# Kernel optimization log

Measured on AMD Instinct MI355X. Metric: run time of the kernel, lower is better.

## Reference

```python
import jax, jax.numpy as jnp
import numpy as np

BETA = 0.9
NORM_EPS = 1e-12  # torch F.normalize default eps


def _sqdist(u, v):
    # ||u||^2 + ||v||^2 - 2 u v^T  (matches module's dist())
    return (u ** 2).sum(1, keepdims=True) + (v ** 2).sum(1) - 2.0 * u @ v.T


def setup_inputs() -> dict:
    key = jax.random.key(0)
    k1, k2 = jax.random.split(key)
    z = jax.random.normal(k1, (16, 4096, 128), dtype=jnp.float32)
    # codebook: unit-norm rows (Hypersphere.random_uniform init)
    w = jax.random.normal(k2, (1024, 128), dtype=jnp.float32)
    emb_w = w / jnp.linalg.norm(w, axis=1, keepdims=True)
    return {"z": z, "emb_w": emb_w}


def reference(z, emb_w):
    B, N, D = z.shape
    n_e = emb_w.shape[0]
    zf = z.reshape(-1, D)  # [B*N, D]

    # codebook self-distances + stats
    cd = _sqdist(emb_w, emb_w)                      # [n_e, n_e]
    min_distance = jnp.sort(cd, axis=0)[1]          # kthvalue(cd, 2, dim=0)
    mean_cb_distance = min_distance.mean()
    mean_cb_variance = jnp.var(cd, axis=1, ddof=1).mean()  # torch.var unbiased

    # quantisation: argmin over codebook
    d = _sqdist(zf, emb_w)                          # [B*N, n_e]
    idx = jnp.argmin(d, axis=1)                     # [B*N]
    z_q = emb_w[idx].reshape(z.shape)               # [B, N, D]

    # F.normalize default dim=1 applied to the 3D tensor -> normalize over N axis
    zn = z_q / jnp.maximum(jnp.linalg.norm(z_q, axis=1, keepdims=True), NORM_EPS)

    sg = jax.lax.stop_gradient
    # legacy loss
    loss = jnp.mean((sg(z_q) - z) ** 2) + BETA * jnp.mean((z_q - sg(z)) ** 2)

    # straight-through estimator
    z_q_st = z + sg(z_q - z)

    # sampled_idx buffer of length B*n_e, scatter 1s at the encoding indices
    sampled_idx = jnp.zeros(B * n_e, dtype=z.dtype).at[idx].set(1.0).reshape(B, n_e)

    si = idx.reshape(B, N)
    return (z_q_st, loss, sampled_idx, idx.reshape(B, -1),
            mean_cb_variance, mean_cb_distance, si, zn)
```

## Files before the change

### kernel.cpp

```cpp
#include <hip/hip_runtime.h>
#include <math.h>

#define D       128
#define NE      1024
#define NROWS   65536
#define NB      16

#define OUT_ZQ    0
#define OUT_LOSS  8388608
#define OUT_SAMP  8388609
#define OUT_IDX   8404993
#define OUT_VAR   8470529
#define OUT_DIST  8470530
#define OUT_SI    8470531
#define OUT_ZN    8536067

#define SCR       8536068
#define SCR_WL    (SCR + 65536)
#define SCR_CNT   (SCR + 131072)
#define SCR_LIST  (SCR + 131073)

#define WS_IDX    0
#define WS_WW     65536
#define WS_FLAGS  66560
#define WS_MIN2   67584
#define WS_VAR    68608
#define WS_LOSSP  69632
#define WS_COLSQP 70144
#define WS_COLSQ  135680

#define MARGIN 2e-3f

typedef __attribute__((ext_vector_type(8))) short s16x8;
typedef __attribute__((ext_vector_type(4))) float f32x4;

#define GLDS16(gp, lp)                                                        \
  __builtin_amdgcn_global_load_lds(                                           \
      (const __attribute__((address_space(1))) unsigned int*)(gp),            \
      (__attribute__((address_space(3))) unsigned int*)(lp), 16, 0, 0)

__device__ __forceinline__ unsigned short f2bf(float f) {
  unsigned int u = __float_as_uint(f);
  return (unsigned short)((u + 0x7FFFu + ((u >> 16) & 1u)) >> 16);
}
__device__ __forceinline__ float bf2f(unsigned short h) {
  return __uint_as_float(((unsigned int)h) << 16);
}

__device__ __forceinline__ float npsq_sum128(const float* p) {
  float a[8];
#pragma unroll
  for (int m = 0; m < 8; ++m) a[m] = __fmul_rn(p[m], p[m]);
  for (int k = 8; k < 128; k += 8) {
#pragma unroll
    for (int m = 0; m < 8; ++m) a[m] = __fadd_rn(a[m], __fmul_rn(p[k + m], p[k + m]));
  }
  float s01 = __fadd_rn(a[0], a[1]);
  float s23 = __fadd_rn(a[2], a[3]);
  float s45 = __fadd_rn(a[4], a[5]);
  float s67 = __fadd_rn(a[6], a[7]);
  return __fadd_rn(__fadd_rn(s01, s23), __fadd_rn(s45, s67));
}

__global__ __launch_bounds__(256) void k_wsplit(const float* __restrict__ w,
                                                float* __restrict__ out,
                                                float* __restrict__ ws) {
  int u = blockIdx.x * 256 + threadIdx.x;
  int c = u >> 4, j = u & 15;
  const float4* p = (const float4*)(w + c * D + j * 8);
  float4 f0 = p[0], f1 = p[1];
  float ff[8] = {f0.x, f0.y, f0.z, f0.w, f1.x, f1.y, f1.z, f1.w};
  s16x8 h, l;
#pragma unroll
  for (int e = 0; e < 8; ++e) {
    unsigned short hb = f2bf(ff[e]);
    h[e] = (short)hb;
    l[e] = (short)f2bf(ff[e] - bf2f(hb));
  }
  unsigned int by = ((unsigned int)(c * 256 + j * 16)) ^ ((unsigned int)((c & 15) << 4));
  *(s16x8*)((char*)(out + SCR) + by)    = h;
  *(s16x8*)((char*)(out + SCR_WL) + by) = l;
  if (u < NE) {
    ws[WS_WW + u] = npsq_sum128(w + u * D);
    ((int*)ws)[WS_FLAGS + u] = 0;
  }
  if (u == 0) ((int*)out)[SCR_CNT] = 0;
}

__global__ __launch_bounds__(256) void k_cb(const float* __restrict__ w,
                                            float* __restrict__ wsf,
                                            float* __restrict__ out) {
  __shared__ float cm1[4][16], cm2[4][16], cS[4][16], cQ[4][16];
  const int t    = threadIdx.x;
  const int lane = t & 63;
  const int wq   = t >> 6;
  const int n    = lane & 15;
  const int q    = lane >> 4;
  const int i0   = blockIdx.x * 16;

  const char* whg = (const char*)(out + SCR);
  const char* wlg = (const char*)(out + SCR_WL);

  s16x8 AH[4], AL[4];
  {
    const float* wr = w + (size_t)(i0 + n) * D;
#pragma unroll
    for (int ks = 0; ks < 4; ++ks) {
      float4 f0 = *(const float4*)(wr + ks * 32 + q * 8);
      float4 f1 = *(const float4*)(wr + ks * 32 + q * 8 + 4);
      float ff[8] = {f0.x, f0.y, f0.z, f0.w, f1.x, f1.y, f1.z, f1.w};
      s16x8 h, l;
#pragma unroll
      for (int j = 0; j < 8; ++j) {
        unsigned short hb = f2bf(ff[j]);
        h[j] = (short)hb;
        l[j] = (short)f2bf(ff[j] - bf2f(hb));
      }
      AH[ks] = h; AL[ks] = l;
    }
  }
  float wwi[4];
#pragma unroll
  for (int r = 0; r < 4; ++r) wwi[r] = wsf[WS_WW + i0 + q * 4 + r];

  float m1[4], m2[4], S[4], Q[4];
#pragma unroll
  for (int r = 0; r < 4; ++r) { m1[r] = INFINITY; m2[r] = INFINITY; S[r] = 0.f; Q[r] = 0.f; }

  for (int ct = 0; ct < 16; ++ct) {
    const int c = wq * 256 + ct * 16 + n;
    const float wwj = wsf[WS_WW + c];
    f32x4 aX = (f32x4){0.f, 0.f, 0.f, 0.f};
    f32x4 aY = (f32x4){0.f, 0.f, 0.f, 0.f};
#pragma unroll
    for (int ks = 0; ks < 4; ++ks) {
      unsigned int off = (unsigned int)(c * 256) +
                         (((unsigned int)(64 * ks + 16 * q)) ^ ((unsigned int)((c & 15) << 4)));
      s16x8 BH = *(const s16x8*)(whg + off);
      s16x8 BL = *(const s16x8*)(wlg + off);
      aX = __builtin_amdgcn_mfma_f32_16x16x32_bf16(AH[ks], BH, aX, 0, 0, 0);
      aY = __builtin_amdgcn_mfma_f32_16x16x32_bf16(AH[ks], BL, aY, 0, 0, 0);
      aY = __builtin_amdgcn_mfma_f32_16x16x32_bf16(AL[ks], BH, aY, 0, 0, 0);
    }
#pragma unroll
    for (int r = 0; r < 4; ++r) {
      float dot = aX[r] + aY[r];
      float d = __fsub_rn(__fadd_rn(wwi[r], wwj), __fmul_rn(2.f, dot));
      if (d < m1[r]) { m2[r] = m1[r]; m1[r] = d; } else m2[r] = fminf(m2[r], d);
      S[r] += d; Q[r] = fmaf(d, d, Q[r]);
    }
  }

#pragma unroll
  for (int r = 0; r < 4; ++r) {
    float a1 = m1[r], a2 = m2[r], s = S[r], qq = Q[r];
#pragma unroll
    for (int mask = 1; mask < 16; mask <<= 1) {
      float b1 = __shfl_xor(a1, mask, 64);
      float b2 = __shfl_xor(a2, mask, 64);
      float bs = __shfl_xor(s,  mask, 64);
      float bq = __shfl_xor(qq, mask, 64);
      a2 = fminf(fminf(a2, b2), fmaxf(a1, b1));
      a1 = fminf(a1, b1);
      s += bs; qq += bq;
    }
    if (n == 0) {
      int rl = q * 4 + r;
      cm1[wq][rl] = a1; cm2[wq][rl] = a2; cS[wq][rl] = s; cQ[wq][rl] = qq;
    }
  }
  __syncthreads();
  if (t < 16) {
    float a1 = cm1[0][t], a2 = cm2[0][t], s = cS[0][t], qq = cQ[0][t];
#pragma unroll
    for (int v = 1; v < 4; ++v) {
      float b1 = cm1[v][t], b2 = cm2[v][t];
      a2 = fminf(fminf(a2, b2), fmaxf(a1, b1));
      a1 = fminf(a1, b1);
      s += cS[v][t]; qq += cQ[v][t];
    }
    wsf[WS_MIN2 + i0 + t] = a2;
    wsf[WS_VAR + i0 + t] = (qq - s * s / (float)NE) / (float)(NE - 1);
  }
}

__global__ __launch_bounds__(512, 2) void k_qmfma(const float* __restrict__ z,
                                                  float* __restrict__ wsf,
                                                  float* __restrict__ out) {
  __shared__ unsigned short Lw[2][16384];
  __shared__ float Lww[1024];
  const int t    = threadIdx.x;
  const int lane = t & 63;
  const int wq   = t >> 6;
  const int n    = lane & 15;
  const int q    = lane >> 4;
  const int rowb = blockIdx.x * 256 + wq * 32;

  const unsigned short* whg = (const unsigned short*)(out + SCR);
  const unsigned short* wlg = (const unsigned short*)(out + SCR_WL);

#define QSTAGE(BUF, P) do {                                              \
    const unsigned short* _wh = whg + (size_t)(P) * 8192;                \
    const unsigned short* _wl = wlg + (size_t)(P) * 8192;                \
    _Pragma("unroll")                                                    \
    for (int _it = 0; _it < 2; ++_it) {                                  \
      int _ci = _it * 512 + t;                                           \
      GLDS16(_wh + _ci * 8, &Lw[BUF][_ci * 8]);                          \
      GLDS16(_wl + _ci * 8, &Lw[BUF][8192 + _ci * 8]);                   \
    } } while (0)

  QSTAGE(0, 0);
  for (int i = t; i < 1024; i += 512) Lww[i] = wsf[WS_WW + i];

  s16x8 AH[2][4], AL[2][4];
#pragma unroll
  for (int rt = 0; rt < 2; ++rt) {
    const float* zr = z + (size_t)(rowb + rt * 16 + n) * D;
#pragma unroll
    for (int ks = 0; ks < 4; ++ks) {
      float4 f0 = *(const float4*)(zr + ks * 32 + q * 8);
      float4 f1 = *(const float4*)(zr + ks * 32 + q * 8 + 4);
      float ff[8] = {f0.x, f0.y, f0.z, f0.w, f1.x, f1.y, f1.z, f1.w};
      s16x8 h, l;
#pragma unroll
      for (int j = 0; j < 8; ++j) {
        unsigned short hb = f2bf(ff[j]);
        h[j] = (short)hb;
        l[j] = (short)f2bf(ff[j] - bf2f(hb));
      }
      AH[rt][ks] = h; AL[rt][ks] = l;
    }
  }

  float m1[2][4], m2[2][4]; int i1[2][4];
#pragma unroll
  for (int rt = 0; rt < 2; ++rt)
#pragma unroll
    for (int r = 0; r < 4; ++r) { m1[rt][r] = INFINITY; m2[rt][r] = INFINITY; i1[rt][r] = 0; }

  __syncthreads();

  for (int p = 0; p < 16; ++p) {
    const int buf = p & 1;
    if (p < 15) QSTAGE(buf ^ 1, p + 1);

    for (int ct = 0; ct < 4; ++ct) {
      const int cL = ct * 16 + n;
      const int c  = p * 64 + cL;
      const float wwc = Lww[c];
      f32x4 aX[2], aY[2];
#pragma unroll
      for (int rt = 0; rt < 2; ++rt) {
        aX[rt] = (f32x4){0.f, 0.f, 0.f, 0.f};
        aY[rt] = (f32x4){0.f, 0.f, 0.f, 0.f};
      }
#pragma unroll
      for (int ks = 0; ks < 4; ++ks) {
        unsigned int off = (unsigned int)(cL * 256) +
                           (((unsigned int)(64 * ks + 16 * q)) ^ ((unsigned int)(cL & 15) << 4));
        s16x8 BH = *(const s16x8*)((const char*)&Lw[buf][0] + off);
        s16x8 BL = *(const s16x8*)((const char*)&Lw[buf][8192] + off);
#pragma unroll
        for (int rt = 0; rt < 2; ++rt) {
          aX[rt] = __builtin_amdgcn_mfma_f32_16x16x32_bf16(AH[rt][ks], BH, aX[rt], 0, 0, 0);
          aY[rt] = __builtin_amdgcn_mfma_f32_16x16x32_bf16(AH[rt][ks], BL, aY[rt], 0, 0, 0);
          aY[rt] = __builtin_amdgcn_mfma_f32_16x16x32_bf16(AL[rt][ks], BH, aY[rt], 0, 0, 0);
        }
      }
#pragma unroll
      for (int rt = 0; rt < 2; ++rt)
#pragma unroll
        for (int r = 0; r < 4; ++r) {
          float v = fmaf(-2.f, aX[rt][r] + aY[rt][r], wwc);
          if (v < m1[rt][r]) { m2[rt][r] = m1[rt][r]; m1[rt][r] = v; i1[rt][r] = c; }
          else m2[rt][r] = fminf(m2[rt][r], v);
        }
    }
    __syncthreads();
  }

#pragma unroll
  for (int rt = 0; rt < 2; ++rt)
#pragma unroll
    for (int r = 0; r < 4; ++r) {
      float a1 = m1[rt][r], a2 = m2[rt][r]; int ai = i1[rt][r];
#pragma unroll
      for (int mask = 1; mask < 16; mask <<= 1) {
        float b1 = __shfl_xor(a1, mask, 64);
        float b2 = __shfl_xor(a2, mask, 64);
        int   bi = __shfl_xor(ai, mask, 64);
        a2 = fminf(fminf(a2, b2), fmaxf(a1, b1));
        bool take = (b1 < a1) || (b1 == a1 && bi < ai);
        a1 = take ? b1 : a1; ai = take ? bi : ai;
      }
      if (n == 0) {
        int grow = rowb + rt * 16 + q * 4 + r;
        if (a2 - a1 > MARGIN) {
          ((int*)wsf)[WS_IDX + grow] = ai;
          out[OUT_IDX + grow] = (float)ai;
          out[OUT_SI  + grow] = (float)ai;
          ((int*)wsf)[WS_FLAGS + ai] = 1;
        } else {
          int pos = atomicAdd(((int*)out) + SCR_CNT, 1);
          ((int*)out)[SCR_LIST + pos] = grow;
        }
      }
    }
#undef QSTAGE
}

__global__ __launch_bounds__(256) void k_fallback(const float* __restrict__ z,
                                                  const float* __restrict__ w,
                                                  float* __restrict__ wsf,
                                                  float* __restrict__ out) {
  const int t = threadIdx.x;
  const int count = ((const int*)out)[SCR_CNT];
  const int* list = ((const int*)out) + SCR_LIST;
  __shared__ float zrow[128];
  __shared__ float zzs;
  __shared__ float rv[256];
  __shared__ int   ri[256];
  for (int i = blockIdx.x; i < count; i += gridDim.x) {
    int row = list[i];
    __syncthreads();
    if (t < 32) ((float4*)zrow)[t] = ((const float4*)(z + (size_t)row * D))[t];
    __syncthreads();
    if (t < 8) {
      float a = __fmul_rn(zrow[t], zrow[t]);
#pragma unroll
      for (int k = 8; k < 128; k += 8)
        a = __fadd_rn(a, __fmul_rn(zrow[k + t], zrow[k + t]));
      float s1 = __fadd_rn(a,  __shfl_xor(a, 1, 64));
      float s2 = __fadd_rn(s1, __shfl_xor(s1, 2, 64));
      float s3 = __fadd_rn(s2, __shfl_xor(s2, 4, 64));
      if (t == 0) zzs = s3;
    }
    __syncthreads();
    float zz = zzs;
    float bv = INFINITY; int bi = 0;
    const float4* z4 = (const float4*)zrow;
    for (int cc = 0; cc < 4; ++cc) {
      int c = cc * 256 + t;
      const float4* wp = (const float4*)(w + (size_t)c * D);
      float acc = 0.f;
#pragma unroll
      for (int k4 = 0; k4 < 32; ++k4) {
        float4 a = wp[k4];
        float4 zv = z4[k4];
        acc = fmaf(zv.x, a.x, acc); acc = fmaf(zv.y, a.y, acc);
        acc = fmaf(zv.z, a.z, acc); acc = fmaf(zv.w, a.w, acc);
      }
      float d = __fsub_rn(__fadd_rn(zz, wsf[WS_WW + c]), __fmul_rn(2.f, acc));
      if (d < bv) { bv = d; bi = c; }
    }
    rv[t] = bv; ri[t] = bi;
    __syncthreads();
    for (int s = 128; s > 0; s >>= 1) {
      if (t < s) {
        float v2 = rv[t + s]; int i2 = ri[t + s];
        if (v2 < rv[t] || (v2 == rv[t] && i2 < ri[t])) { rv[t] = v2; ri[t] = i2; }
      }
      __syncthreads();
    }
    if (t == 0) {
      int mi = ri[0];
      ((int*)wsf)[WS_IDX + row] = mi;
      out[OUT_IDX + row] = (float)mi;
      out[OUT_SI  + row] = (float)mi;
      ((int*)wsf)[WS_FLAGS + mi] = 1;
    }
  }
}

__global__ __launch_bounds__(256) void k_gather(const float* __restrict__ z,
                                                const float* __restrict__ w,
                                                float* __restrict__ ws,
                                                float* __restrict__ out) {
  __shared__ float csp[32][8][4];
  __shared__ float lred[256];
  const int t = threadIdx.x, blk = blockIdx.x;
  const int c4 = t & 31, rg = t >> 5;
  float lp = 0.f;
  float csx = 0.f, csy = 0.f, csz = 0.f, csw = 0.f;
  for (int m = 0; m < 16; ++m) {
    int r  = rg + 8 * m;
    int gr = blk * 128 + r;
    int idx = ((const int*)ws)[WS_IDX + gr];
    float4 qv = *(const float4*)&w[idx * D + c4 * 4];
    float4 zv = *(const float4*)&z[(size_t)gr * D + c4 * 4];
    *(float4*)&out[OUT_ZQ + (size_t)gr * D + c4 * 4] = qv;
    float dx = qv.x - zv.x, dy = qv.y - zv.y, dz = qv.z - zv.z, dw = qv.w - zv.w;
    lp = fmaf(dx, dx, lp); lp = fmaf(dy, dy, lp);
    lp = fmaf(dz, dz, lp); lp = fmaf(dw, dw, lp);
    csx = fmaf(qv.x, qv.x, csx); csy = fmaf(qv.y, qv.y, csy);
    csz = fmaf(qv.z, qv.z, csz); csw = fmaf(qv.w, qv.w, csw);
  }
  csp[c4][rg][0] = csx; csp[c4][rg][1] = csy;
  csp[c4][rg][2] = csz; csp[c4][rg][3] = csw;
  lred[t] = lp;
  __syncthreads();
  for (int s = 128; s > 0; s >>= 1) {
    if (t < s) lred[t] += lred[t + s];
    __syncthreads();
  }
  if (t == 0) ws[WS_LOSSP + blk] = lred[0];
  if (t < 128) {
    int dcol = t;
    float s = 0.f;
    for (int g = 0; g < 8; ++g) s += csp[dcol >> 2][g][dcol & 3];
    ws[WS_COLSQP + blk * 128 + dcol] = s;
  }
}

__global__ __launch_bounds__(256) void k_zn(const float* __restrict__ ws,
                                            const float* __restrict__ w,
                                            float* __restrict__ out) {
  const int t = threadIdx.x, blk = blockIdx.x;
  const int c4 = t & 31, rg = t >> 5;
  const int b = blk >> 5;
  float csx = 0.f, csy = 0.f, csz = 0.f, csw = 0.f;
  for (int rb = 0; rb < 32; ++rb) {
    float4 pp = *(const float4*)&ws[WS_COLSQP + (size_t)(b * 32 + rb) * 128 + c4 * 4];
    csx += pp.x; csy += pp.y; csz += pp.z; csw += pp.w;
  }
  float nx = fmaxf(sqrtf(csx), 1e-12f);
  float ny = fmaxf(sqrtf(csy), 1e-12f);
  float nz = fmaxf(sqrtf(csz), 1e-12f);
  float nw = fmaxf(sqrtf(csw), 1e-12f);
  for (int m = 0; m < 16; ++m) {
    int gr = blk * 128 + rg + 8 * m;
    int idx = ((const int*)ws)[WS_IDX + gr];
    float4 qv = *(const float4*)&w[idx * D + c4 * 4];
    size_t o = (size_t)gr * D + c4 * 4;
    out[OUT_ZN + o + 0] = qv.x / nx;
    out[OUT_ZN + o + 1] = qv.y / ny;
    out[OUT_ZN + o + 2] = qv.z / nz;
    out[OUT_ZN + o + 3] = qv.w / nw;
  }
  if (blk == 0) {
    __shared__ float f1[256], f2[256], f3[256];
    __syncthreads();
    f1[t] = ws[WS_LOSSP + t] + ws[WS_LOSSP + t + 256];
    f2[t] = (ws[WS_MIN2 + t] + ws[WS_MIN2 + t + 512]) +
            (ws[WS_MIN2 + t + 256] + ws[WS_MIN2 + t + 768]);
    f3[t] = (ws[WS_VAR + t] + ws[WS_VAR + t + 512]) +
            (ws[WS_VAR + t + 256] + ws[WS_VAR + t + 768]);
    __syncthreads();
    for (int s = 128; s > 0; s >>= 1) {
      if (t < s) { f1[t] += f1[t + s]; f2[t] += f2[t + s]; f3[t] += f3[t + s]; }
      __syncthreads();
    }
    if (t == 0) {
      float m = f1[0] / 8388608.f;
      out[OUT_LOSS] = m + 0.9f * m;
      out[OUT_VAR]  = f3[0] / 1024.f;
      out[OUT_DIST] = f2[0] / 1024.f;
    }
    const int* flags = (const int*)ws + WS_FLAGS;
    for (int i = t; i < NB * NE; i += 256)
      out[OUT_SAMP + i] = (i < NE && flags[i] != 0) ? 1.f : 0.f;
  }
}

extern "C" void kernel_launch(void* const* d_in, const int* in_sizes, int n_in,
                              void* d_out, int out_size, void* d_ws, size_t ws_size,
                              hipStream_t stream) {
  const float* z = (const float*)d_in[0];
  const float* w = (const float*)d_in[1];
  float* out = (float*)d_out;
  float* ws  = (float*)d_ws;

  hipLaunchKernelGGL(k_wsplit,   dim3(64),   dim3(256), 0, stream, w, out, ws);
  hipLaunchKernelGGL(k_cb,       dim3(64),   dim3(256), 0, stream, w, ws, out);
  hipLaunchKernelGGL(k_qmfma,    dim3(256),  dim3(512), 0, stream, z, ws, out);
  hipLaunchKernelGGL(k_fallback, dim3(1024), dim3(256), 0, stream, z, w, ws, out);
  hipLaunchKernelGGL(k_gather,   dim3(512),  dim3(256), 0, stream, z, w, ws, out);
  hipLaunchKernelGGL(k_zn,       dim3(512),  dim3(256), 0, stream, ws, w, out);
}
```

Measured before the change: 140.5 us.

## Read codebook from global in quantizer and fold fallback into gather kernel

The quantizer kernel stops staging the split bf16 codebook into LDS with double buffering. It now reads B fragments straight from global memory, relying on L2/L1 caching, and runs 256-thread blocks over 128 rows each. Ambiguous rows are marked with idx=-1 instead of being appended to a global atomic list. The separate fallback kernel is removed and its exact recompute now runs inside the gather kernel per 128-row block, saving one launch and the global atomic counter. The trade-off is more global and cache traffic in the MFMA inner loop, and ambiguous rows are serialized per block in gather.

```diff
diff --git a/kernel.cpp b/kernel.cpp
--- a/kernel.cpp
+++ b/kernel.cpp
@@ -17,8 +17,6 @@
 
 #define SCR       8536068
 #define SCR_WL    (SCR + 65536)
-#define SCR_CNT   (SCR + 131072)
-#define SCR_LIST  (SCR + 131073)
 
 #define WS_IDX    0
 #define WS_WW     65536
@@ -27,17 +25,11 @@
 #define WS_VAR    68608
 #define WS_LOSSP  69632
 #define WS_COLSQP 70144
-#define WS_COLSQ  135680
 
 #define MARGIN 2e-3f
 
 typedef __attribute__((ext_vector_type(8))) short s16x8;
 typedef __attribute__((ext_vector_type(4))) float f32x4;
-
-#define GLDS16(gp, lp)                                                        \
-  __builtin_amdgcn_global_load_lds(                                           \
-      (const __attribute__((address_space(1))) unsigned int*)(gp),            \
-      (__attribute__((address_space(3))) unsigned int*)(lp), 16, 0, 0)
 
 __device__ __forceinline__ unsigned short f2bf(float f) {
   unsigned int u = __float_as_uint(f);
@@ -84,7 +76,6 @@
     ws[WS_WW + u] = npsq_sum128(w + u * D);
     ((int*)ws)[WS_FLAGS + u] = 0;
   }
-  if (u == 0) ((int*)out)[SCR_CNT] = 0;
 }
 
 __global__ __launch_bounds__(256) void k_cb(const float* __restrict__ w,
@@ -184,33 +175,18 @@
   }
 }
 
-__global__ __launch_bounds__(512, 2) void k_qmfma(const float* __restrict__ z,
+__global__ __launch_bounds__(256, 2) void k_qmfma(const float* __restrict__ z,
                                                   float* __restrict__ wsf,
                                                   float* __restrict__ out) {
-  __shared__ unsigned short Lw[2][16384];
-  __shared__ float Lww[1024];
   const int t    = threadIdx.x;
   const int lane = t & 63;
   const int wq   = t >> 6;
   const int n    = lane & 15;
   const int q    = lane >> 4;
-  const int rowb = blockIdx.x * 256 + wq * 32;
-
-  const unsigned short* whg = (const unsigned short*)(out + SCR);
-  const unsigned short* wlg = (const unsigned short*)(out + SCR_WL);
-
-#define QSTAGE(BUF, P) do {                                              \
-    const unsigned short* _wh = whg + (size_t)(P) * 8192;                \
-    const unsigned short* _wl = wlg + (size_t)(P) * 8192;                \
-    _Pragma("unroll")                                                    \
-    for (int _it = 0; _it < 2; ++_it) {                                  \
-      int _ci = _it * 512 + t;                                           \
-      GLDS16(_wh + _ci * 8, &Lw[BUF][_ci * 8]);                          \
-      GLDS16(_wl + _ci * 8, &Lw[BUF][8192 + _ci * 8]);                   \
-    } } while (0)
-
-  QSTAGE(0, 0);
-  for (int i = t; i < 1024; i += 512) Lww[i] = wsf[WS_WW + i];
+  const int rowb = blockIdx.x * 128 + wq * 32;
+
+  const char* whg = (const char*)(out + SCR);
+  const char* wlg = (const char*)(out + SCR_WL);
 
   s16x8 AH[2][4], AL[2][4];
 #pragma unroll
@@ -238,45 +214,36 @@
 #pragma unroll
     for (int r = 0; r < 4; ++r) { m1[rt][r] = INFINITY; m2[rt][r] = INFINITY; i1[rt][r] = 0; }
 
-  __syncthreads();
-
-  for (int p = 0; p < 16; ++p) {
-    const int buf = p & 1;
-    if (p < 15) QSTAGE(buf ^ 1, p + 1);
-
-    for (int ct = 0; ct < 4; ++ct) {
-      const int cL = ct * 16 + n;
-      const int c  = p * 64 + cL;
-      const float wwc = Lww[c];
-      f32x4 aX[2], aY[2];
+  for (int ct = 0; ct < 64; ++ct) {
+    const int c = ct * 16 + n;
+    const float wwc = wsf[WS_WW + c];
+    f32x4 aX[2], aY[2];
+#pragma unroll
+    for (int rt = 0; rt < 2; ++rt) {
+      aX[rt] = (f32x4){0.f, 0.f, 0.f, 0.f};
+      aY[rt] = (f32x4){0.f, 0.f, 0.f, 0.f};
+    }
+#pragma unroll
+    for (int ks = 0; ks < 4; ++ks) {
+      unsigned int off = (unsigned int)(c * 256) +
+                         (((unsigned int)(64 * ks + 16 * q)) ^ ((unsigned int)((c & 15) << 4)));
+      s16x8 BH = *(const s16x8*)(whg + off);
+      s16x8 BL = *(const s16x8*)(wlg + off);
 #pragma unroll
       for (int rt = 0; rt < 2; ++rt) {
-        aX[rt] = (f32x4){0.f, 0.f, 0.f, 0.f};
-        aY[rt] = (f32x4){0.f, 0.f, 0.f, 0.f};
-      }
-#pragma unroll
-      for (int ks = 0; ks < 4; ++ks) {
-        unsigned int off = (unsigned int)(cL * 256) +
-                           (((unsigned int)(64 * ks + 16 * q)) ^ ((unsigned int)(cL & 15) << 4));
-        s16x8 BH = *(const s16x8*)((const char*)&Lw[buf][0] + off);
-        s16x8 BL = *(const s16x8*)((const char*)&Lw[buf][8192] + off);
-#pragma unroll
-        for (int rt = 0; rt < 2; ++rt) {
-          aX[rt] = __builtin_amdgcn_mfma_f32_16x16x32_bf16(AH[rt][ks], BH, aX[rt], 0, 0, 0);
-          aY[rt] = __builtin_amdgcn_mfma_f32_16x16x32_bf16(AH[rt][ks], BL, aY[rt], 0, 0, 0);
-          aY[rt] = __builtin_amdgcn_mfma_f32_16x16x32_bf16(AL[rt][ks], BH, aY[rt], 0, 0, 0);
-        }
-      }
-#pragma unroll
-      for (int rt = 0; rt < 2; ++rt)
-#pragma unroll
-        for (int r = 0; r < 4; ++r) {
-          float v = fmaf(-2.f, aX[rt][r] + aY[rt][r], wwc);
-          if (v < m1[rt][r]) { m2[rt][r] = m1[rt][r]; m1[rt][r] = v; i1[rt][r] = c; }
-          else m2[rt][r] = fminf(m2[rt][r], v);
-        }
-    }
-    __syncthreads();
+        aX[rt] = __builtin_amdgcn_mfma_f32_16x16x32_bf16(AH[rt][ks], BH, aX[rt], 0, 0, 0);
+        aY[rt] = __builtin_amdgcn_mfma_f32_16x16x32_bf16(AH[rt][ks], BL, aY[rt], 0, 0, 0);
+        aY[rt] = __builtin_amdgcn_mfma_f32_16x16x32_bf16(AL[rt][ks], BH, aY[rt], 0, 0, 0);
+      }
+    }
+#pragma unroll
+    for (int rt = 0; rt < 2; ++rt)
+#pragma unroll
+      for (int r = 0; r < 4; ++r) {
+        float v = fmaf(-2.f, aX[rt][r] + aY[rt][r], wwc);
+        if (v < m1[rt][r]) { m2[rt][r] = m1[rt][r]; m1[rt][r] = v; i1[rt][r] = c; }
+        else m2[rt][r] = fminf(m2[rt][r], v);
+      }
   }
 
 #pragma unroll
@@ -301,27 +268,37 @@
           out[OUT_SI  + grow] = (float)ai;
           ((int*)wsf)[WS_FLAGS + ai] = 1;
         } else {
-          int pos = atomicAdd(((int*)out) + SCR_CNT, 1);
-          ((int*)out)[SCR_LIST + pos] = grow;
+          ((int*)wsf)[WS_IDX + grow] = -1;
         }
       }
     }
-#undef QSTAGE
-}
-
-__global__ __launch_bounds__(256) void k_fallback(const float* __restrict__ z,
-                                                  const float* __restrict__ w,
-                                                  float* __restrict__ wsf,
-                                                  float* __restrict__ out) {
-  const int t = threadIdx.x;
-  const int count = ((const int*)out)[SCR_CNT];
-  const int* list = ((const int*)out) + SCR_LIST;
+}
+
+__global__ __launch_bounds__(256) void k_gather(const float* __restrict__ z,
+                                                const float* __restrict__ w,
+                                                float* __restrict__ ws,
+                                                float* __restrict__ out) {
+  __shared__ float csp[32][8][4];
+  __shared__ float lred[256];
+  __shared__ int   fcnt;
+  __shared__ int   frows[128];
   __shared__ float zrow[128];
   __shared__ float zzs;
   __shared__ float rv[256];
   __shared__ int   ri[256];
-  for (int i = blockIdx.x; i < count; i += gridDim.x) {
-    int row = list[i];
+  const int t = threadIdx.x, blk = blockIdx.x;
+
+  if (t == 0) fcnt = 0;
+  __syncthreads();
+  if (t < 128) {
+    if (((const int*)ws)[WS_IDX + blk * 128 + t] < 0) {
+      int p = atomicAdd(&fcnt, 1);
+      frows[p] = blk * 128 + t;
+    }
+  }
+  __syncthreads();
+  for (int i = 0; i < fcnt; ++i) {
+    int row = frows[i];
     __syncthreads();
     if (t < 32) ((float4*)zrow)[t] = ((const float4*)(z + (size_t)row * D))[t];
     __syncthreads();
@@ -350,7 +327,7 @@
         acc = fmaf(zv.x, a.x, acc); acc = fmaf(zv.y, a.y, acc);
         acc = fmaf(zv.z, a.z, acc); acc = fmaf(zv.w, a.w, acc);
       }
-      float d = __fsub_rn(__fadd_rn(zz, wsf[WS_WW + c]), __fmul_rn(2.f, acc));
+      float d = __fsub_rn(__fadd_rn(zz, ws[WS_WW + c]), __fmul_rn(2.f, acc));
       if (d < bv) { bv = d; bi = c; }
     }
     rv[t] = bv; ri[t] = bi;
@@ -364,21 +341,14 @@
     }
     if (t == 0) {
       int mi = ri[0];
-      ((int*)wsf)[WS_IDX + row] = mi;
+      ((int*)ws)[WS_IDX + row] = mi;
       out[OUT_IDX + row] = (float)mi;
       out[OUT_SI  + row] = (float)mi;
-      ((int*)wsf)[WS_FLAGS + mi] = 1;
-    }
-  }
-}
-
-__global__ __launch_bounds__(256) void k_gather(const float* __restrict__ z,
-                                                const float* __restrict__ w,
-                                                float* __restrict__ ws,
-                                                float* __restrict__ out) {
-  __shared__ float csp[32][8][4];
-  __shared__ float lred[256];
-  const int t = threadIdx.x, blk = blockIdx.x;
+      ((int*)ws)[WS_FLAGS + mi] = 1;
+    }
+  }
+  __syncthreads();
+
   const int c4 = t & 31, rg = t >> 5;
   float lp = 0.f;
   float csx = 0.f, csy = 0.f, csz = 0.f, csw = 0.f;
@@ -470,10 +440,9 @@
   float* out = (float*)d_out;
   float* ws  = (float*)d_ws;
 
-  hipLaunchKernelGGL(k_wsplit,   dim3(64),   dim3(256), 0, stream, w, out, ws);
-  hipLaunchKernelGGL(k_cb,       dim3(64),   dim3(256), 0, stream, w, ws, out);
-  hipLaunchKernelGGL(k_qmfma,    dim3(256),  dim3(512), 0, stream, z, ws, out);
-  hipLaunchKernelGGL(k_fallback, dim3(1024), dim3(256), 0, stream, z, w, ws, out);
-  hipLaunchKernelGGL(k_gather,   dim3(512),  dim3(256), 0, stream, z, w, ws, out);
-  hipLaunchKernelGGL(k_zn,       dim3(512),  dim3(256), 0, stream, ws, w, out);
-}
+  hipLaunchKernelGGL(k_wsplit, dim3(64),  dim3(256), 0, stream, w, out, ws);
+  hipLaunchKernelGGL(k_cb,     dim3(64),  dim3(256), 0, stream, w, ws, out);
+  hipLaunchKernelGGL(k_qmfma,  dim3(512), dim3(256), 0, stream, z, ws, out);
+  hipLaunchKernelGGL(k_gather, dim3(512), dim3(256), 0, stream, z, w, ws, out);
+  hipLaunchKernelGGL(k_zn,     dim3(512), dim3(256), 0, stream, ws, w, out);
+}
```

Result: slower. 202.1 us (+43.8%).
